# Kernel tuning notes

Hardware: AMD Instinct MI355X
Metric: run time of the kernel (lower is better)

The kernel has to match this reference:

```python
import jax, jax.numpy as jnp
import numpy as np


def setup_inputs() -> dict:
    key = jax.random.key(0)
    k_h, k_w1, k_w2 = jax.random.split(key, 3)
    B, S, D = 8, 2048, 1024
    H = 2 * D  # reasoning_net hidden width
    # xavier_uniform-style scaled weights
    lim1 = float(np.sqrt(6.0 / (D + H)))
    lim2 = float(np.sqrt(6.0 / (H + D)))
    return {
        "hidden_states": jax.random.normal(k_h, (B, S, D), dtype=jnp.float32),
        "W1": jax.random.uniform(k_w1, (D, H), dtype=jnp.float32, minval=-lim1, maxval=lim1),
        "b1": jnp.zeros((H,), dtype=jnp.float32),
        "W2": jax.random.uniform(k_w2, (H, D), dtype=jnp.float32, minval=-lim2, maxval=lim2),
        "b2": jnp.zeros((D,), dtype=jnp.float32),
    }


def reference(hidden_states, W1, b1, W2, b2):
    """Chain reasoning forward.

    The torch loop carries output[:, -1:], but reasoning_net is a per-token MLP
    (Linear over the last dim), so processed[:, -1:] == MLP(current token) and the
    carried state never influences appended outputs. Faithful closed form:
      out[:, 0]  = hidden_states[:, 0]
      out[:, i]  = MLP(hidden_states[:, i])  for i >= 1
    Dropout is identity (eval). GELU is exact (torch default).
    """
    rest = hidden_states[:, 1:, :]  # [B, S-1, D]
    h = jax.nn.gelu(jnp.einsum("bsd,dh->bsh", rest, W1) + b1, approximate=False)
    out_rest = jnp.einsum("bsh,hd->bsd", h, W2) + b2
    return jnp.concatenate([hidden_states[:, :1, :], out_rest], axis=1)
```

## Files before the change

kernel.cpp:

```cpp
#include <hip/hip_runtime.h>
#include <cstdint>
#include <cstddef>

typedef unsigned short u16;
typedef __attribute__((ext_vector_type(8))) __bf16 bf16x8;
typedef __attribute__((ext_vector_type(8))) unsigned short u16x8;
typedef __attribute__((ext_vector_type(4))) unsigned short u16x4;
typedef __attribute__((ext_vector_type(4))) float f32x4;

__device__ __forceinline__ void gload_lds16(const void* g, void* l) {
    __builtin_amdgcn_global_load_lds(
        (const __attribute__((address_space(1))) unsigned int*)g,
        (__attribute__((address_space(3))) unsigned int*)l,
        16, 0, 0);
}

__device__ __forceinline__ u16 f2bf(float f) {
    union { float f; unsigned int u; } v; v.f = f;
    unsigned int r = v.u + 0x7fffu + ((v.u >> 16) & 1u);
    return (u16)(r >> 16);
}

__device__ __forceinline__ float gelu_tanh(float x) {
    const float z = 0.7978845608028654f * x * (1.0f + 0.044715f * x * x);
    const float t = __builtin_amdgcn_exp2f(2.885390081777927f * z);
    const float th = 1.0f - 2.0f * __builtin_amdgcn_rcpf(t + 1.0f);
    return 0.5f * x * (1.0f + th);
}


#define STAGE(mb, hrow, kb, lbase)                                   \
    {                                                                \
        const char* _s = (mb) + (size_t)(hrow)*ldb + (kb);           \
        gload_lds16(_s + soff[0], smem + (lbase) + ldst[0]);         \
        gload_lds16(_s + soff[1], smem + (lbase) + ldst[1]);         \
    }
#define LOADA(bufo, mh)                                              \
    _Pragma("unroll") for (int ks = 0; ks < 2; ++ks) {               \
        const char* _p = smem + (bufo) + A0 + g2[ks] + (mh)*8192;    \
        _Pragma("unroll") for (int m = 0; m < 4; ++m)                \
            af[m][ks] = *(const bf16x8*)(_p + m * 2048);             \
    }
#define LOADB(bufo, nh)                                              \
    _Pragma("unroll") for (int ks = 0; ks < 2; ++ks) {               \
        const char* _p = smem + (bufo) + 32768 + B0 + g2[ks] + (nh)*4096; \
        _Pragma("unroll") for (int n = 0; n < 2; ++n)                \
            bf[(nh)*2 + n][ks] = *(const bf16x8*)(_p + n * 2048);    \
    }
#define QMFMA(MS, NS)                                                \
    __builtin_amdgcn_s_setprio(1);                                   \
    _Pragma("unroll") for (int ks = 0; ks < 2; ++ks)                 \
    _Pragma("unroll") for (int m = 0; m < 4; ++m)                    \
    _Pragma("unroll") for (int n = 0; n < 2; ++n)                    \
        acc[(MS) + m][(NS) + n] = __builtin_amdgcn_mfma_f32_16x16x32_bf16( \
            af[m][ks], bf[(NS) + n][ks], acc[(MS) + m][(NS) + n], 0, 0, 0); \
    __builtin_amdgcn_s_setprio(0);
#define BAR __builtin_amdgcn_s_barrier()
#define SB0 __builtin_amdgcn_sched_barrier(0)
#define LGKM0                                                        \
    {                                                                \
        asm volatile("s_waitcnt lgkmcnt(0)" ::: "memory");           \
        SB0;                                                         \
    }

template <int GELU, int OUT_BF16, int SKIP_S>
__global__ __launch_bounds__(512, 2) void gemm256(
    const u16* __restrict__ A, const u16* __restrict__ Bt,
    const float* __restrict__ bias, void* __restrict__ Cv,
    int N, int K, int row0) {
    __shared__ __align__(16) char smem[131072];

    const int tid = threadIdx.x, lane = tid & 63, wave = tid >> 6;
    const int wr = wave >> 2, wc = wave & 3;
    const int mrow = lane & 15, half = lane >> 4;

    const size_t ldb = (size_t)K * 2;
    const char* Ab = (const char*)A + (size_t)blockIdx.x * 256 * ldb;
    const char* Bb = (const char*)Bt + (size_t)blockIdx.y * 256 * ldb;

    size_t soff[2];
    int ldst[2];
#pragma unroll
    for (int i = 0; i < 2; ++i) {
        const int L = tid + 512 * i, r = L >> 3, s = L & 7;
        soff[i] = (size_t)r * ldb + (size_t)((s ^ (r & 7)) << 4);
        ldst[i] = L << 4;
    }

    const int A0 = (wr * 128 + mrow) * 128;
    const int B0 = (wc * 64 + mrow) * 128;
    int g2[2];
#pragma unroll
    for (int ks = 0; ks < 2; ++ks) g2[ks] = ((ks * 4 + half) ^ (mrow & 7)) << 4;

    f32x4 acc[8][4];
#pragma unroll
    for (int i = 0; i < 8; ++i)
#pragma unroll
        for (int j = 0; j < 4; ++j) acc[i][j] = f32x4{0.f, 0.f, 0.f, 0.f};

    bf16x8 af[4][2], bf[4][2];

    STAGE(Ab, 0, 0, 0)
    STAGE(Ab, 128, 0, 16384)
    STAGE(Bb, 0, 0, 32768)
    STAGE(Bb, 128, 0, 49152)
    STAGE(Bb, 0, 128, 98304)
    STAGE(Bb, 128, 0 + 128, 114688)
    asm volatile("s_waitcnt vmcnt(4)" ::: "memory");
    SB0;
    BAR;
    SB0;

    const int niter = K >> 7;
    for (int it = 0; it < niter; ++it) {
        const bool last = (it == niter - 1);
        const size_t kb1 = (size_t)(2 * it + 1) << 7;
        const size_t kb2 = kb1 + 128, kb3 = kb1 + 256;
        LOADA(0, 0)
        LOADB(0, 0)
        STAGE(Ab, 0, kb1, 65536)
        BAR;
        LGKM0
        QMFMA(0, 0)
        BAR;
        LOADB(0, 1)
        STAGE(Ab, 128, kb1, 81920)
        BAR;
        LGKM0
        QMFMA(0, 2)
        BAR;
        LOADA(0, 1)
        if (!last) STAGE(Bb, 0, kb2, 32768)
        BAR;
        LGKM0
        QMFMA(4, 0)
        BAR;
        if (!last) STAGE(Bb, 128, kb2, 49152)
        BAR;
        QMFMA(4, 2)
        if (last) {
            asm volatile("s_waitcnt vmcnt(0)" ::: "memory");
        } else {
            asm volatile("s_waitcnt vmcnt(4)" ::: "memory");
        }
        SB0;
        BAR;
        SB0;
        LOADA(65536, 0)
        LOADB(65536, 0)
        if (!last) STAGE(Ab, 0, kb2, 0)
        BAR;
        LGKM0
        QMFMA(0, 0)
        BAR;
        LOADB(65536, 1)
        if (!last) STAGE(Ab, 128, kb2, 16384)
        BAR;
        LGKM0
        QMFMA(0, 2)
        BAR;
        LOADA(65536, 1)
        if (!last) STAGE(Bb, 0, kb3, 98304)
        BAR;
        LGKM0
        QMFMA(4, 0)
        BAR;
        if (!last) STAGE(Bb, 128, kb3, 114688)
        BAR;
        QMFMA(4, 2)
        if (!last) asm volatile("s_waitcnt vmcnt(4)" ::: "memory");
        SB0;
        BAR;
        SB0;
    }

    const int growbase = blockIdx.x * 256, gcolbase = blockIdx.y * 256;
    float* Ct = (float*)smem;
    const int rr = tid >> 3, gb = tid & 7, r7 = rr & 7;
#pragma unroll
    for (int c = 0; c < 4; ++c) {
        __syncthreads();
        if (wr == (c >> 1)) {
#pragma unroll
            for (int dm = 0; dm < 4; ++dm) {
                const int mi = (c & 1) * 4 + dm;
#pragma unroll
                for (int ni = 0; ni < 4; ++ni) {
                    const int col = wc * 64 + ni * 16 + mrow;
                    const float bv = bias[gcolbase + col];
#pragma unroll
                    for (int r = 0; r < 4; ++r) {
                        const int rloc = dm * 16 + half * 4 + r;
                        float v = acc[mi][ni][r] + bv;
                        if (GELU) v = gelu_tanh(v);
                        Ct[rloc * 256 +
                           ((((col >> 2) ^ (rloc & 7)) << 2) | (col & 3))] = v;
                    }
                }
            }
        }
        __syncthreads();
        const int grow = growbase + 64 * c + rr;
        if (!(SKIP_S && (((row0 + grow) & 2047) == 0))) {
            f32x4 v[8];
#pragma unroll
            for (int j = 0; j < 8; ++j)
                v[j] = *(const f32x4*)(Ct + rr * 256 +
                                       (((gb ^ r7) + 8 * j) << 2));
            if (OUT_BF16) {
                u16* p = (u16*)Cv + (size_t)grow * N + gcolbase + gb * 4;
#pragma unroll
                for (int j = 0; j < 8; ++j) {
                    u16x4 o;
#pragma unroll
                    for (int e = 0; e < 4; ++e) o[e] = f2bf(v[j][e]);
                    *(u16x4*)(p + 32 * j) = o;
                }
            } else {
                float* p = (float*)Cv + (size_t)grow * N + gcolbase + gb * 4;
#pragma unroll
                for (int j = 0; j < 8; ++j) *(f32x4*)(p + 32 * j) = v[j];
            }
        }
    }
}

__device__ __forceinline__ void tcvt_block(const float* __restrict__ src,
                                           u16* __restrict__ dst, int R, int C,
                                           int bx, int by, int x, int y,
                                           u16 (*t)[33]) {
    for (int i = 0; i < 32; i += 8)
        t[y + i][x] = f2bf(src[(size_t)(by + y + i) * C + (bx + x)]);
    __syncthreads();
    for (int i = 0; i < 32; i += 8)
        dst[(size_t)(bx + y + i) * R + (by + x)] = t[x][y + i];
}

__global__ void prep(const float* __restrict__ X, const float* __restrict__ W1,
                     const float* __restrict__ W2, u16* __restrict__ Xb,
                     u16* __restrict__ W1T, u16* __restrict__ W2T,
                     float* __restrict__ out, long long nX) {
    __shared__ u16 t[32][33];
    const int b = blockIdx.x, tid = threadIdx.x;
    const int x = tid & 31, y = tid >> 5;
    if (b < 2048) {
        tcvt_block(W1, W1T, 1024, 2048, (b & 63) * 32, (b >> 6) * 32, x, y, t);
    } else if (b < 4096) {
        const int bi = b - 2048;
        tcvt_block(W2, W2T, 2048, 1024, (bi & 31) * 32, (bi >> 5) * 32, x, y, t);
    } else if (b < 4104) {
        const size_t base = (size_t)(b - 4096) * 2048 * 1024;
        *(float4*)(out + base + tid * 4) = *(const float4*)(X + base + tid * 4);
    } else {
        const long long stride = (long long)4096 * 256 * 4;
        for (long long i = ((long long)(b - 4104) * 256 + tid) * 4; i < nX;
             i += stride) {
            const float4 v = *(const float4*)(X + i);
            ushort4 o;
            o.x = f2bf(v.x); o.y = f2bf(v.y); o.z = f2bf(v.z); o.w = f2bf(v.w);
            *(ushort4*)(Xb + i) = o;
        }
    }
}

extern "C" void kernel_launch(void* const* d_in, const int* in_sizes, int n_in,
                              void* d_out, int out_size, void* d_ws, size_t ws_size,
                              hipStream_t stream) {
    const float* X  = (const float*)d_in[0];
    const float* W1 = (const float*)d_in[1];
    const float* b1 = (const float*)d_in[2];
    const float* W2 = (const float*)d_in[3];
    const float* b2 = (const float*)d_in[4];
    float* out = (float*)d_out;

    const int B = 8, S = 2048, D = 1024, H = 2048;
    const int M = B * S;

    u16* W1T = (u16*)d_ws;
    u16* W2T = W1T + (size_t)H * D;
    u16* Xb  = W2T + (size_t)D * H;
    u16* Hb  = Xb + (size_t)M * D;
    const size_t wfixed = (size_t)H * D * 2 * 2 + (size_t)M * D * 2;
    size_t avail_rows = (ws_size > wfixed) ? (ws_size - wfixed) / ((size_t)H * 2) : 0;
    int CM = (int)((avail_rows / 256) * 256);
    if (CM > M) CM = M;
    if (CM < 256) CM = 256;

    prep<<<dim3(8200), dim3(256), 0, stream>>>(
        X, W1, W2, Xb, W1T, W2T, out, (long long)M * D);

    for (int m0 = 0; m0 < M; m0 += CM) {
        const int rows = (M - m0 < CM) ? (M - m0) : CM;
        dim3 g1(rows / 256, H / 256);
        gemm256<1, 1, 0><<<g1, dim3(512), 0, stream>>>(
            Xb + (size_t)m0 * D, W1T, b1, Hb, H, D, m0);
        dim3 g2(rows / 256, D / 256);
        gemm256<0, 0, 1><<<g2, dim3(512), 0, stream>>>(
            Hb, W2T, b2, out + (size_t)m0 * D, D, H, m0);
    }
}
```

Measured before the change: 282.6 us.

## Prefetch A tiles a full stage ahead and fence barriers with sched_barrier

```diff
diff --git a/kernel.cpp b/kernel.cpp
--- a/kernel.cpp
+++ b/kernel.cpp
@@ -57,6 +57,7 @@
     __builtin_amdgcn_s_setprio(0);
 #define BAR __builtin_amdgcn_s_barrier()
 #define SB0 __builtin_amdgcn_sched_barrier(0)
+#define VMC(n) asm volatile("s_waitcnt vmcnt(" #n ")" ::: "memory")
 #define LGKM0                                                        \
     {                                                                \
         asm volatile("s_waitcnt lgkmcnt(0)" ::: "memory");           \
@@ -106,8 +107,10 @@
     STAGE(Bb, 0, 0, 32768)
     STAGE(Bb, 128, 0, 49152)
     STAGE(Bb, 0, 128, 98304)
-    STAGE(Bb, 128, 0 + 128, 114688)
-    asm volatile("s_waitcnt vmcnt(4)" ::: "memory");
+    STAGE(Bb, 128, 128, 114688)
+    STAGE(Ab, 0, 128, 65536)
+    STAGE(Ab, 128, 128, 81920)
+    VMC(8);
     SB0;
     BAR;
     SB0;
@@ -115,64 +118,60 @@
     const int niter = K >> 7;
     for (int it = 0; it < niter; ++it) {
         const bool last = (it == niter - 1);
-        const size_t kb1 = (size_t)(2 * it + 1) << 7;
-        const size_t kb2 = kb1 + 128, kb3 = kb1 + 256;
+        const size_t kb2 = (size_t)(2 * it + 2) << 7;
+        const size_t kb3 = kb2 + 128;
         LOADA(0, 0)
         LOADB(0, 0)
-        STAGE(Ab, 0, kb1, 65536)
-        BAR;
+        SB0; BAR;
         LGKM0
         QMFMA(0, 0)
-        BAR;
+        SB0; BAR;
         LOADB(0, 1)
-        STAGE(Ab, 128, kb1, 81920)
-        BAR;
+        SB0; BAR;
         LGKM0
         QMFMA(0, 2)
-        BAR;
+        SB0; BAR;
         LOADA(0, 1)
         if (!last) STAGE(Bb, 0, kb2, 32768)
-        BAR;
+        SB0; BAR;
         LGKM0
         QMFMA(4, 0)
-        BAR;
-        if (!last) STAGE(Bb, 128, kb2, 49152)
-        BAR;
+        SB0; BAR;
+        if (!last) {
+            STAGE(Bb, 128, kb2, 49152)
+            STAGE(Ab, 0, kb2, 0)
+            STAGE(Ab, 128, kb2, 16384)
+        }
+        SB0; BAR;
         QMFMA(4, 2)
-        if (last) {
-            asm volatile("s_waitcnt vmcnt(0)" ::: "memory");
-        } else {
-            asm volatile("s_waitcnt vmcnt(4)" ::: "memory");
-        }
-        SB0;
-        BAR;
-        SB0;
+        if (last) VMC(0); else VMC(8);
+        SB0; BAR; SB0;
         LOADA(65536, 0)
         LOADB(65536, 0)
-        if (!last) STAGE(Ab, 0, kb2, 0)
-        BAR;
+        SB0; BAR;
         LGKM0
         QMFMA(0, 0)
-        BAR;
+        SB0; BAR;
         LOADB(65536, 1)
-        if (!last) STAGE(Ab, 128, kb2, 16384)
-        BAR;
+        SB0; BAR;
         LGKM0
         QMFMA(0, 2)
-        BAR;
+        SB0; BAR;
         LOADA(65536, 1)
         if (!last) STAGE(Bb, 0, kb3, 98304)
-        BAR;
+        SB0; BAR;
         LGKM0
         QMFMA(4, 0)
-        BAR;
-        if (!last) STAGE(Bb, 128, kb3, 114688)
-        BAR;
+        SB0; BAR;
+        if (!last) {
+            STAGE(Bb, 128, kb3, 114688)
+            STAGE(Ab, 0, kb3, 65536)
+            STAGE(Ab, 128, kb3, 81920)
+        }
+        SB0; BAR;
         QMFMA(4, 2)
-        if (!last) asm volatile("s_waitcnt vmcnt(4)" ::: "memory");
-        SB0;
-        BAR;
-        SB0;
+        if (last) VMC(0); else VMC(8);
+        SB0; BAR; SB0;
     }
 
     const int growbase = blockIdx.x * 256, gcolbase = blockIdx.y * 256;
```

Result: no change. 284.6 us (+0.7%).
